# Kernel tuning notes

Measured on AMD Instinct MI355X. Metric: run time of the kernel, lower is better.

The kernel has to match this reference:

```python
import jax, jax.numpy as jnp
import numpy as np

DATA_DIM = 2048
COORD_DIM = 2
NUM_V = DATA_DIM // COORD_DIM  # 1024 vertices
HID = 256
TDIM = 128
NUM_LAYERS = 4
B = 512


def _sinusoidal(t, dim=TDIM):
    half = dim // 2
    freqs = jnp.exp(-jnp.log(10000.0) * jnp.arange(half, dtype=jnp.float32) / (half - 1))
    ang = t.astype(jnp.float32)[:, None] * freqs[None, :]  # (B, half)
    return jnp.concatenate([jnp.sin(ang), jnp.cos(ang)], axis=1)  # (B, dim)


def _cycle_agg(h):
    # degree-3 cycle graph (self + next + prev), values 1/3 each == circular-shift mean
    # h: (B, V, D)
    return (h + jnp.roll(h, -1, axis=1) + jnp.roll(h, 1, axis=1)) * (1.0 / 3.0)


def setup_inputs() -> dict:
    key = jax.random.key(0)
    ks = jax.random.split(key, 16)
    dims = [COORD_DIM + TDIM] + [HID] * NUM_LAYERS  # [130,256,256,256,256]

    def glorot(k, shape):
        fan_in = shape[0]
        return jax.random.normal(k, shape, dtype=jnp.float32) / jnp.sqrt(jnp.float32(fan_in))

    inp = {
        'x': jax.random.normal(ks[0], (B, DATA_DIM), dtype=jnp.float32),
        't': jax.random.randint(ks[1], (B,), 0, 1000, dtype=jnp.int32),
        'time_W': glorot(ks[2], (TDIM, TDIM)),
        'time_b': jnp.zeros((TDIM,), jnp.float32),
        'W0': glorot(ks[3], (dims[0], dims[1])), 'b0': jnp.zeros((dims[1],), jnp.float32),
        'W1': glorot(ks[4], (dims[1], dims[2])), 'b1': jnp.zeros((dims[2],), jnp.float32),
        'W2': glorot(ks[5], (dims[2], dims[3])), 'b2': jnp.zeros((dims[3],), jnp.float32),
        'W3': glorot(ks[6], (dims[3], dims[4])), 'b3': jnp.zeros((dims[4],), jnp.float32),
        'res0_W': glorot(ks[7], (dims[0], dims[1])),
        'hW1': glorot(ks[8], (HID, HID)), 'hb1': jnp.zeros((HID,), jnp.float32),
        'hW2': glorot(ks[9], (HID, COORD_DIM)), 'hb2': jnp.zeros((COORD_DIM,), jnp.float32),
    }
    return inp


def reference(x, t, time_W, time_b, W0, b0, W1, b1, W2, b2, W3, b3, res0_W, hW1, hb1, hW2, hb2):
    silu = jax.nn.silu
    coords = x.reshape(B, NUM_V, COORD_DIM)
    temb = silu(_sinusoidal(t) @ time_W + time_b)  # (B, TDIM)
    temb = jnp.broadcast_to(temb[:, None, :], (B, NUM_V, TDIM))
    h = jnp.concatenate([coords, temb], axis=-1)  # (B, V, 130)

    Ws = [W0, W1, W2, W3]
    bs = [b0, b1, b2, b3]
    for i in range(NUM_LAYERS):
        residual = h @ res0_W if i == 0 else h
        # GraphConvolution: adj @ (h W) + b, with adj == normalized cycle aggregation
        h = _cycle_agg(h @ Ws[i]) + bs[i] + residual
        h = silu(h)

    h = silu(h @ hW1 + hb1) @ hW2 + hb2  # (B, V, 2)
    return h.reshape(B, DATA_DIM)
```

## Files before the change

### kernel.cpp

```cpp
#include <hip/hip_runtime.h>


typedef __attribute__((ext_vector_type(8))) short bf16x8;
typedef __attribute__((ext_vector_type(4))) float f32x4;

#define NV 1024

#define OFF_W0T   0
#define OFF_W1T   40960
#define OFF_W2T   106496
#define OFF_W3T   172032
#define OFF_HW1T  237568
#define OFF_HW2T  303104
#define OFF_TEMB  307200
#define PREP_ELEMS 307200

__device__ __forceinline__ float bf2f(short u){
  union { unsigned int i; float f; } v;
  v.i = ((unsigned int)(unsigned short)u) << 16;
  return v.f;
}
__device__ __forceinline__ short f2bf(float f){
  union { float f; unsigned int i; } v; v.f = f;
  unsigned int r = v.i + 0x7FFFu + ((v.i >> 16) & 1u);
  return (short)(r >> 16);
}
__device__ __forceinline__ float silu_f(float v){
  float e = __expf(-v);
  return v * __builtin_amdgcn_rcpf(1.f + e);
}
__device__ __forceinline__ f32x4 zero4(){ f32x4 z = {0.f,0.f,0.f,0.f}; return z; }

__global__ void prep_kernel(const float* __restrict__ W0, const float* __restrict__ res0,
                            const float* __restrict__ W1, const float* __restrict__ W2,
                            const float* __restrict__ W3, const float* __restrict__ hW1,
                            const float* __restrict__ hW2, short* __restrict__ ws){
  int idx = blockIdx.x * 256 + threadIdx.x;
  if (idx >= PREP_ELEMS) return;
  float v = 0.f;
  if (idx < 40960){
    int n = idx / 160, k = idx - n * 160;
    if (k < 128)      v = W0[(k + 2) * 256 + n] + res0[(k + 2) * 256 + n];
    else if (k < 130) v = W0[(k - 128) * 256 + n];
    else if (k < 132) v = res0[(k - 130) * 256 + n];
  } else if (idx < 303104){
    int rem = idx - 40960;
    int seg = rem >> 16;
    int r2 = rem & 65535;
    int n = r2 >> 8, k = r2 & 255;
    const float* src = (seg == 0) ? W1 : (seg == 1) ? W2 : (seg == 2) ? W3 : hW1;
    v = src[k * 256 + n];
  } else {
    int rem = idx - 303104;
    int n = rem >> 8, k = rem & 255;
    if (n < 2) v = hW2[k * 2 + n];
  }
  ws[idx] = f2bf(v);
}

__global__ void temb_kernel(const int* __restrict__ t, const float* __restrict__ tW,
                            const float* __restrict__ tb, short* __restrict__ temb){
  __shared__ float sc[128];
  int b = blockIdx.x, n = threadIdx.x;
  float tv = (float)t[b];
  {
    int j = n & 63;
    float fr = __expf(-9.210340371976184f * (float)j * (1.f / 63.f));
    float ang = tv * fr;
    sc[n] = (n < 64) ? sinf(ang) : cosf(ang);
  }
  __syncthreads();
  float acc = tb[n];
  #pragma unroll 8
  for (int k = 0; k < 128; ++k) acc += sc[k] * tW[k * 128 + n];
  temb[b * 128 + n] = f2bf(silu_f(acc));
}

template<int KPAD>
__device__ __forceinline__ void mm4(const char* hb, const short* __restrict__ Wt,
                                    int m15, int g, int n0, f32x4 acc[5][4]){
  const short* wb = Wt + (n0 + m15) * KPAD + g * 8;
  #pragma unroll 2
  for (int ks = 0; ks < KPAD / 32; ++ks){
    bf16x8 bf[4];
    #pragma unroll
    for (int nt = 0; nt < 4; ++nt)
      bf[nt] = *(const bf16x8*)(wb + nt * 16 * KPAD + ks * 32);
    const int kb = ks * 64 + g * 16;
    #pragma unroll
    for (int mt = 0; mt < 5; ++mt){
      const int row = mt * 16 + m15;
      bf16x8 a = *(const bf16x8*)(hb + row * 512 + (kb ^ ((row & 7) << 4)));
      #pragma unroll
      for (int nt = 0; nt < 4; ++nt)
        acc[mt][nt] = __builtin_amdgcn_mfma_f32_16x16x32_bf16(a, bf[nt], acc[mt][nt], 0, 0, 0);
    }
  }
}

__global__ __launch_bounds__(256, 2)
void gcn_fused(const float* __restrict__ x, const short* __restrict__ ws,
               const float* __restrict__ b0p, const float* __restrict__ b1p,
               const float* __restrict__ b2p, const float* __restrict__ b3p,
               const float* __restrict__ hb1p, const float* __restrict__ hb2p,
               float* __restrict__ out){
  extern __shared__ char hb[];
  const int tid = threadIdx.x;
  const int lane = tid & 63, wid = tid >> 6;
  const int m15 = lane & 15, g = lane >> 4;
  const int n0 = wid * 64;
  const int b = blockIdx.y, v0 = blockIdx.x * 64;

  {
    const short* tembp = ws + OFF_TEMB + b * 128;
    for (int task = tid; task < 72 * 16; task += 256){
      int r = task >> 4, ck = (task & 15) * 16;
      *(bf16x8*)(hb + r * 512 + (ck ^ ((r & 7) << 4))) =
          *(const bf16x8*)(tembp + (task & 15) * 8);
    }
    for (int task = tid; task < 80 * 8; task += 256){
      int r = task >> 3, q = task & 7;
      bf16x8 v = {0, 0, 0, 0, 0, 0, 0, 0};
      if (q == 0 && r < 72){
        const float* xb = x + b * 2048;
        int vm = (v0 + r - 5) & (NV - 1);
        int vc = (v0 + r - 4) & (NV - 1);
        int vp = (v0 + r - 3) & (NV - 1);
        float c0m = xb[vm * 2], c1m = xb[vm * 2 + 1];
        float c0c = xb[vc * 2], c1c = xb[vc * 2 + 1];
        float c0p = xb[vp * 2], c1p = xb[vp * 2 + 1];
        v[0] = f2bf((c0m + c0c + c0p) * (1.f / 3.f));
        v[1] = f2bf((c1m + c1c + c1p) * (1.f / 3.f));
        v[2] = f2bf(c0c);
        v[3] = f2bf(c1c);
      }
      *(bf16x8*)(hb + r * 512 + (((16 + q) * 16) ^ ((r & 7) << 4))) = v;
    }
  }
  __syncthreads();

  f32x4 acc[5][4];

  {
    #pragma unroll
    for (int mt = 0; mt < 5; ++mt)
      #pragma unroll
      for (int nt = 0; nt < 4; ++nt) acc[mt][nt] = zero4();
    mm4<160>(hb, ws + OFF_W0T, m15, g, n0, acc);
    __syncthreads();
    const float bias[4] = { b0p[n0 + m15], b0p[n0 + 16 + m15],
                            b0p[n0 + 32 + m15], b0p[n0 + 48 + m15] };
    #pragma unroll
    for (int mt = 0; mt < 5; ++mt)
      #pragma unroll
      for (int nt = 0; nt < 4; ++nt){
        const int row = mt * 16 + g * 4;
        const int cb = (n0 + nt * 16 + m15) * 2;
        #pragma unroll
        for (int j = 0; j < 4; ++j){
          short q = f2bf(silu_f(acc[mt][nt][j] + bias[nt]));
          *(short*)(hb + (row + j) * 512 + (cb ^ (((row + j) & 7) << 4))) = q;
        }
      }
  }
  __syncthreads();

  #pragma unroll
  for (int L = 0; L < 3; ++L){
    const short* Wt = ws + (L == 0 ? OFF_W1T : L == 1 ? OFF_W2T : OFF_W3T);
    const float* bp = (L == 0 ? b1p : L == 1 ? b2p : b3p);
    #pragma unroll
    for (int mt = 0; mt < 5; ++mt)
      #pragma unroll
      for (int nt = 0; nt < 4; ++nt) acc[mt][nt] = zero4();
    mm4<256>(hb, Wt, m15, g, n0, acc);
    __syncthreads();
    const float bias[4] = { bp[n0 + m15], bp[n0 + 16 + m15],
                            bp[n0 + 32 + m15], bp[n0 + 48 + m15] };
    #pragma unroll
    for (int mt = 0; mt < 5; ++mt)
      #pragma unroll
      for (int nt = 0; nt < 4; ++nt){
        float a0 = acc[mt][nt][0], a1 = acc[mt][nt][1];
        float a2 = acc[mt][nt][2], a3 = acc[mt][nt][3];
        float upv = (g == 3) ? acc[mt > 0 ? mt - 1 : 0][nt][3] : a3;
        float pm0 = __shfl(upv, (lane + 48) & 63);
        float dnv = (g == 0) ? acc[mt < 4 ? mt + 1 : 4][nt][0] : a0;
        float pp3 = __shfl(dnv, (lane + 16) & 63);
        float base = bias[nt];
        const int row = mt * 16 + g * 4;
        const int cb = (n0 + nt * 16 + m15) * 2;
        float r0 = bf2f(*(const short*)(hb + (row    ) * 512 + (cb ^ (((row    ) & 7) << 4))));
        float r1 = bf2f(*(const short*)(hb + (row + 1) * 512 + (cb ^ (((row + 1) & 7) << 4))));
        float r2 = bf2f(*(const short*)(hb + (row + 2) * 512 + (cb ^ (((row + 2) & 7) << 4))));
        float r3 = bf2f(*(const short*)(hb + (row + 3) * 512 + (cb ^ (((row + 3) & 7) << 4))));
        float s0 = (pm0 + a0 + a1) * (1.f / 3.f) + base + r0;
        float s1 = (a0 + a1 + a2) * (1.f / 3.f) + base + r1;
        float s2 = (a1 + a2 + a3) * (1.f / 3.f) + base + r2;
        float s3 = (a2 + a3 + pp3) * (1.f / 3.f) + base + r3;
        *(short*)(hb + (row    ) * 512 + (cb ^ (((row    ) & 7) << 4))) = f2bf(silu_f(s0));
        *(short*)(hb + (row + 1) * 512 + (cb ^ (((row + 1) & 7) << 4))) = f2bf(silu_f(s1));
        *(short*)(hb + (row + 2) * 512 + (cb ^ (((row + 2) & 7) << 4))) = f2bf(silu_f(s2));
        *(short*)(hb + (row + 3) * 512 + (cb ^ (((row + 3) & 7) << 4))) = f2bf(silu_f(s3));
      }
    __syncthreads();
  }

  {
    #pragma unroll
    for (int mt = 0; mt < 5; ++mt)
      #pragma unroll
      for (int nt = 0; nt < 4; ++nt) acc[mt][nt] = zero4();
    mm4<256>(hb, ws + OFF_HW1T, m15, g, n0, acc);
    __syncthreads();
    const float bias[4] = { hb1p[n0 + m15], hb1p[n0 + 16 + m15],
                            hb1p[n0 + 32 + m15], hb1p[n0 + 48 + m15] };
    #pragma unroll
    for (int mt = 0; mt < 5; ++mt)
      #pragma unroll
      for (int nt = 0; nt < 4; ++nt){
        const int row = mt * 16 + g * 4;
        const int cb = (n0 + nt * 16 + m15) * 2;
        #pragma unroll
        for (int j = 0; j < 4; ++j){
          short q = f2bf(silu_f(acc[mt][nt][j] + bias[nt]));
          *(short*)(hb + (row + j) * 512 + (cb ^ (((row + j) & 7) << 4))) = q;
        }
      }
    __syncthreads();
  }

  if (wid == 0){
    f32x4 a2[5];
    #pragma unroll
    for (int mt = 0; mt < 5; ++mt) a2[mt] = zero4();
    const short* wb = ws + OFF_HW2T + m15 * 256 + g * 8;
    #pragma unroll 2
    for (int ks = 0; ks < 8; ++ks){
      bf16x8 bfr = *(const bf16x8*)(wb + ks * 32);
      const int kb = ks * 64 + g * 16;
      #pragma unroll
      for (int mt = 0; mt < 5; ++mt){
        const int row = mt * 16 + m15;
        bf16x8 a = *(const bf16x8*)(hb + row * 512 + (kb ^ ((row & 7) << 4)));
        a2[mt] = __builtin_amdgcn_mfma_f32_16x16x32_bf16(a, bfr, a2[mt], 0, 0, 0);
      }
    }
    if (m15 < 2){
      float bias = hb2p[m15];
      #pragma unroll
      for (int mt = 0; mt < 5; ++mt)
        #pragma unroll
        for (int j = 0; j < 4; ++j){
          int row = mt * 16 + g * 4 + j;
          if (row >= 4 && row < 68)
            out[b * 2048 + (v0 + row - 4) * 2 + m15] = a2[mt][j] + bias;
        }
    }
  }
}

extern "C" void kernel_launch(void* const* d_in, const int* in_sizes, int n_in,
                              void* d_out, int out_size, void* d_ws, size_t ws_size,
                              hipStream_t stream){
  const float* x   = (const float*)d_in[0];
  const int*   t   = (const int*)  d_in[1];
  const float* tW  = (const float*)d_in[2];
  const float* tb  = (const float*)d_in[3];
  const float* W0  = (const float*)d_in[4];
  const float* b0  = (const float*)d_in[5];
  const float* W1  = (const float*)d_in[6];
  const float* b1  = (const float*)d_in[7];
  const float* W2  = (const float*)d_in[8];
  const float* b2  = (const float*)d_in[9];
  const float* W3  = (const float*)d_in[10];
  const float* b3  = (const float*)d_in[11];
  const float* res0= (const float*)d_in[12];
  const float* hW1 = (const float*)d_in[13];
  const float* hb1 = (const float*)d_in[14];
  const float* hW2 = (const float*)d_in[15];
  const float* hb2 = (const float*)d_in[16];
  short* ws  = (short*)d_ws;
  float* out = (float*)d_out;

  hipFuncSetAttribute((const void*)gcn_fused,
                      hipFuncAttributeMaxDynamicSharedMemorySize, 40960);

  prep_kernel<<<dim3((PREP_ELEMS + 255) / 256), dim3(256), 0, stream>>>(
      W0, res0, W1, W2, W3, hW1, hW2, ws);
  temb_kernel<<<dim3(512), dim3(128), 0, stream>>>(t, tW, tb, ws + OFF_TEMB);
  gcn_fused<<<dim3(16, 512), dim3(256), 40960, stream>>>(
      x, ws, b0, b1, b2, b3, hb1, hb2, out);
}
```

Before: 866.9 us.

## Split fused GCN block across 8 waves and fold 1/3 into weights

Doubles the block size from 256 to 512 threads so each wave computes 32 output columns instead of 64, halving per-wave accumulator registers and raising launch bounds to allow 4 blocks per CU. The 1/3 cycle-aggregation factor is folded into the bf16 layer weights W1-W3 during prep, which removes three multiplies per element in the epilogue. The hand-written bf16 conversions are replaced with HIP library intrinsics. The risk is more barrier participants per block and LDS capacity limits (40KB per block) on how many blocks can actually be co-resident.

Result: faster. 791.2 us (-8.7%).

```diff
diff --git a/kernel.cpp b/kernel.cpp
--- a/kernel.cpp
+++ b/kernel.cpp
@@ -1,4 +1,5 @@
 #include <hip/hip_runtime.h>
+#include <hip/hip_bf16.h>
 
 
 typedef __attribute__((ext_vector_type(8))) short bf16x8;
@@ -16,14 +17,13 @@
 #define PREP_ELEMS 307200
 
 __device__ __forceinline__ float bf2f(short u){
-  union { unsigned int i; float f; } v;
-  v.i = ((unsigned int)(unsigned short)u) << 16;
-  return v.f;
+  __hip_bfloat16 h;
+  *reinterpret_cast<short*>(&h) = u;
+  return __bfloat162float(h);
 }
 __device__ __forceinline__ short f2bf(float f){
-  union { float f; unsigned int i; } v; v.f = f;
-  unsigned int r = v.i + 0x7FFFu + ((v.i >> 16) & 1u);
-  return (short)(r >> 16);
+  __hip_bfloat16 h = __float2bfloat16(f);
+  return *reinterpret_cast<short*>(&h);
 }
 __device__ __forceinline__ float silu_f(float v){
   float e = __expf(-v);
@@ -50,6 +50,7 @@
     int n = r2 >> 8, k = r2 & 255;
     const float* src = (seg == 0) ? W1 : (seg == 1) ? W2 : (seg == 2) ? W3 : hW1;
     v = src[k * 256 + n];
+    if (seg < 3) v *= (1.f / 3.f);
   } else {
     int rem = idx - 303104;
     int n = rem >> 8, k = rem & 255;
@@ -77,28 +78,25 @@
 }
 
 template<int KPAD>
-__device__ __forceinline__ void mm4(const char* hb, const short* __restrict__ Wt,
-                                    int m15, int g, int n0, f32x4 acc[5][4]){
+__device__ __forceinline__ void mm2(const char* hb, const short* __restrict__ Wt,
+                                    int m15, int g, int n0, f32x4 acc[5][2]){
   const short* wb = Wt + (n0 + m15) * KPAD + g * 8;
   #pragma unroll 2
   for (int ks = 0; ks < KPAD / 32; ++ks){
-    bf16x8 bf[4];
-    #pragma unroll
-    for (int nt = 0; nt < 4; ++nt)
-      bf[nt] = *(const bf16x8*)(wb + nt * 16 * KPAD + ks * 32);
+    bf16x8 bf0 = *(const bf16x8*)(wb + ks * 32);
+    bf16x8 bf1 = *(const bf16x8*)(wb + 16 * KPAD + ks * 32);
     const int kb = ks * 64 + g * 16;
     #pragma unroll
     for (int mt = 0; mt < 5; ++mt){
       const int row = mt * 16 + m15;
       bf16x8 a = *(const bf16x8*)(hb + row * 512 + (kb ^ ((row & 7) << 4)));
-      #pragma unroll
-      for (int nt = 0; nt < 4; ++nt)
-        acc[mt][nt] = __builtin_amdgcn_mfma_f32_16x16x32_bf16(a, bf[nt], acc[mt][nt], 0, 0, 0);
-    }
-  }
-}
-
-__global__ __launch_bounds__(256, 2)
+      acc[mt][0] = __builtin_amdgcn_mfma_f32_16x16x32_bf16(a, bf0, acc[mt][0], 0, 0, 0);
+      acc[mt][1] = __builtin_amdgcn_mfma_f32_16x16x32_bf16(a, bf1, acc[mt][1], 0, 0, 0);
+    }
+  }
+}
+
+__global__ __launch_bounds__(512, 4)
 void gcn_fused(const float* __restrict__ x, const short* __restrict__ ws,
                const float* __restrict__ b0p, const float* __restrict__ b1p,
                const float* __restrict__ b2p, const float* __restrict__ b3p,
@@ -108,17 +106,17 @@
   const int tid = threadIdx.x;
   const int lane = tid & 63, wid = tid >> 6;
   const int m15 = lane & 15, g = lane >> 4;
-  const int n0 = wid * 64;
+  const int n0 = wid * 32;
   const int b = blockIdx.y, v0 = blockIdx.x * 64;
 
   {
     const short* tembp = ws + OFF_TEMB + b * 128;
-    for (int task = tid; task < 72 * 16; task += 256){
+    for (int task = tid; task < 72 * 16; task += 512){
       int r = task >> 4, ck = (task & 15) * 16;
       *(bf16x8*)(hb + r * 512 + (ck ^ ((r & 7) << 4))) =
           *(const bf16x8*)(tembp + (task & 15) * 8);
     }
-    for (int task = tid; task < 80 * 8; task += 256){
+    for (int task = tid; task < 80 * 8; task += 512){
       int r = task >> 3, q = task & 7;
       bf16x8 v = {0, 0, 0, 0, 0, 0, 0, 0};
       if (q == 0 && r < 72){
@@ -139,21 +137,18 @@
   }
   __syncthreads();
 
-  f32x4 acc[5][4];
-
-  {
+  f32x4 acc[5][2];
+
+  {
+    #pragma unroll
+    for (int mt = 0; mt < 5; ++mt){ acc[mt][0] = zero4(); acc[mt][1] = zero4(); }
+    mm2<160>(hb, ws + OFF_W0T, m15, g, n0, acc);
+    __syncthreads();
+    const float bias[2] = { b0p[n0 + m15], b0p[n0 + 16 + m15] };
     #pragma unroll
     for (int mt = 0; mt < 5; ++mt)
       #pragma unroll
-      for (int nt = 0; nt < 4; ++nt) acc[mt][nt] = zero4();
-    mm4<160>(hb, ws + OFF_W0T, m15, g, n0, acc);
-    __syncthreads();
-    const float bias[4] = { b0p[n0 + m15], b0p[n0 + 16 + m15],
-                            b0p[n0 + 32 + m15], b0p[n0 + 48 + m15] };
-    #pragma unroll
-    for (int mt = 0; mt < 5; ++mt)
-      #pragma unroll
-      for (int nt = 0; nt < 4; ++nt){
+      for (int nt = 0; nt < 2; ++nt){
         const int row = mt * 16 + g * 4;
         const int cb = (n0 + nt * 16 + m15) * 2;
         #pragma unroll
@@ -170,17 +165,14 @@
     const short* Wt = ws + (L == 0 ? OFF_W1T : L == 1 ? OFF_W2T : OFF_W3T);
     const float* bp = (L == 0 ? b1p : L == 1 ? b2p : b3p);
     #pragma unroll
+    for (int mt = 0; mt < 5; ++mt){ acc[mt][0] = zero4(); acc[mt][1] = zero4(); }
+    mm2<256>(hb, Wt, m15, g, n0, acc);
+    __syncthreads();
+    const float bias[2] = { bp[n0 + m15], bp[n0 + 16 + m15] };
+    #pragma unroll
     for (int mt = 0; mt < 5; ++mt)
       #pragma unroll
-      for (int nt = 0; nt < 4; ++nt) acc[mt][nt] = zero4();
-    mm4<256>(hb, Wt, m15, g, n0, acc);
-    __syncthreads();
-    const float bias[4] = { bp[n0 + m15], bp[n0 + 16 + m15],
-                            bp[n0 + 32 + m15], bp[n0 + 48 + m15] };
-    #pragma unroll
-    for (int mt = 0; mt < 5; ++mt)
-      #pragma unroll
-      for (int nt = 0; nt < 4; ++nt){
+      for (int nt = 0; nt < 2; ++nt){
         float a0 = acc[mt][nt][0], a1 = acc[mt][nt][1];
         float a2 = acc[mt][nt][2], a3 = acc[mt][nt][3];
         float upv = (g == 3) ? acc[mt > 0 ? mt - 1 : 0][nt][3] : a3;
@@ -194,10 +186,10 @@
         float r1 = bf2f(*(const short*)(hb + (row + 1) * 512 + (cb ^ (((row + 1) & 7) << 4))));
         float r2 = bf2f(*(const short*)(hb + (row + 2) * 512 + (cb ^ (((row + 2) & 7) << 4))));
         float r3 = bf2f(*(const short*)(hb + (row + 3) * 512 + (cb ^ (((row + 3) & 7) << 4))));
-        float s0 = (pm0 + a0 + a1) * (1.f / 3.f) + base + r0;
-        float s1 = (a0 + a1 + a2) * (1.f / 3.f) + base + r1;
-        float s2 = (a1 + a2 + a3) * (1.f / 3.f) + base + r2;
-        float s3 = (a2 + a3 + pp3) * (1.f / 3.f) + base + r3;
+        float s0 = pm0 + a0 + a1 + base + r0;
+        float s1 = a0 + a1 + a2 + base + r1;
+        float s2 = a1 + a2 + a3 + base + r2;
+        float s3 = a2 + a3 + pp3 + base + r3;
         *(short*)(hb + (row    ) * 512 + (cb ^ (((row    ) & 7) << 4))) = f2bf(silu_f(s0));
         *(short*)(hb + (row + 1) * 512 + (cb ^ (((row + 1) & 7) << 4))) = f2bf(silu_f(s1));
         *(short*)(hb + (row + 2) * 512 + (cb ^ (((row + 2) & 7) << 4))) = f2bf(silu_f(s2));
@@ -208,17 +200,14 @@
 
   {
     #pragma unroll
+    for (int mt = 0; mt < 5; ++mt){ acc[mt][0] = zero4(); acc[mt][1] = zero4(); }
+    mm2<256>(hb, ws + OFF_HW1T, m15, g, n0, acc);
+    __syncthreads();
+    const float bias[2] = { hb1p[n0 + m15], hb1p[n0 + 16 + m15] };
+    #pragma unroll
     for (int mt = 0; mt < 5; ++mt)
       #pragma unroll
-      for (int nt = 0; nt < 4; ++nt) acc[mt][nt] = zero4();
-    mm4<256>(hb, ws + OFF_HW1T, m15, g, n0, acc);
-    __syncthreads();
-    const float bias[4] = { hb1p[n0 + m15], hb1p[n0 + 16 + m15],
-                            hb1p[n0 + 32 + m15], hb1p[n0 + 48 + m15] };
-    #pragma unroll
-    for (int mt = 0; mt < 5; ++mt)
-      #pragma unroll
-      for (int nt = 0; nt < 4; ++nt){
+      for (int nt = 0; nt < 2; ++nt){
         const int row = mt * 16 + g * 4;
         const int cb = (n0 + nt * 16 + m15) * 2;
         #pragma unroll
@@ -289,6 +278,6 @@
   prep_kernel<<<dim3((PREP_ELEMS + 255) / 256), dim3(256), 0, stream>>>(
       W0, res0, W1, W2, W3, hW1, hW2, ws);
   temb_kernel<<<dim3(512), dim3(128), 0, stream>>>(t, tW, tb, ws + OFF_TEMB);
-  gcn_fused<<<dim3(16, 512), dim3(256), 40960, stream>>>(
+  gcn_fused<<<dim3(16, 512), dim3(512), 40960, stream>>>(
       x, ws, b0, b1, b2, b3, hb1, hb2, out);
 }
```
